# Optimization experiments

Hardware: AMD Instinct MI355X
Metric: run time of the kernel (lower is better)

Reference implementation:

```python
import jax, jax.numpy as jnp
import numpy as np

# Config: b=2, n=1024, dim=512, heads=8, dim_head=64, L=8 slices/head, temperature=0.1

def setup_inputs() -> dict:
    key = jax.random.key(0)
    ks = jax.random.split(key, 5)
    b, n, dim = 2, 1024, 512
    heads, dim_head, L = 8, 64, 8
    inner = heads * dim_head
    x = jax.random.normal(ks[0], (b, n, dim), jnp.float32)
    W_qkv = jax.random.normal(ks[1], (dim, 3 * inner), jnp.float32) * 0.02
    theta = jax.random.normal(ks[2], (heads, L, dim_head), jnp.float32)
    W_out = jax.random.normal(ks[3], (inner, dim), jnp.float32) * 0.02
    b_out = jnp.zeros((dim,), jnp.float32)
    return {"x": x, "W_qkv": W_qkv, "theta": theta, "W_out": W_out, "b_out": b_out}


def reference(x, W_qkv, theta, W_out, b_out):
    b, n, dim = x.shape
    heads, L, dim_head = theta.shape
    scale = dim_head ** -0.5
    temperature = 0.1
    # QKV projection (no bias) and head split: b n (h d) -> b h n d
    qkv = x @ W_qkv
    q, k, v = jnp.split(qkv, 3, axis=-1)
    sh = lambda t: t.reshape(b, n, heads, dim_head).transpose(0, 2, 1, 3)
    q = sh(q) * scale
    k = sh(k) * scale
    v = sh(v)
    # Esp: learnable unit slice directions per head, 1D projections
    th = theta / jnp.linalg.norm(theta, axis=-1, keepdims=True)  # [h, L, d]
    qp = jnp.einsum('bhnd,hld->bhln', q, th)  # [b,h,L,n]
    kp = jnp.einsum('bhnd,hld->bhln', k, th)
    # per-slice soft 1D transport plan (rows sum to 1), averaged over slices,
    # scaled to total-mass-1 plan (rows sum 1/n)
    d2 = (qp[..., :, None] - kp[..., None, :]) ** 2  # [b,h,L,n,n]
    plans = jax.nn.softmax(-d2 / temperature, axis=-1)
    P = plans.mean(axis=2) / n  # [b,h,n,n], rows sum to 1/n
    # SA: attn = attn * attn.shape[-1] -> row-stochastic
    attn = P * n
    out = jnp.einsum('bhnm,bhmd->bhnd', attn, v)
    out = out.transpose(0, 2, 1, 3).reshape(b, n, heads * dim_head)
    out = out @ W_out + b_out  # to_out Linear (dropout=0 in eval)
    return out, attn
```

## Files before the change

### kernel.cpp

```cpp
#include <hip/hip_runtime.h>
#include <hip/hip_bf16.h>

#define CEXP (-14.4269504088896340736f)

typedef __attribute__((ext_vector_type(8))) short bfrag8;
typedef __attribute__((ext_vector_type(4))) float fvec4;
typedef __attribute__((ext_vector_type(8))) unsigned short ushort8;
typedef __attribute__((ext_vector_type(4))) unsigned short ushort4v;

__device__ inline unsigned short f2bf(float f) {
    unsigned u = __builtin_bit_cast(unsigned, f);
    u += 0x7fffu + ((u >> 16) & 1u);
    return (unsigned short)(u >> 16);
}
__device__ inline float bf2f(unsigned short h) {
    unsigned u = ((unsigned)h) << 16;
    return __builtin_bit_cast(float, u);
}

template <int CTRL, int RMASK>
__device__ __forceinline__ float dpp_add(float v) {
    int m = __builtin_amdgcn_update_dpp(0, __builtin_bit_cast(int, v), CTRL, RMASK, 0xf, true);
    return v + __builtin_bit_cast(float, m);
}
__device__ __forceinline__ float wave_sum64(float v) {
    v = dpp_add<0xB1,  0xf>(v);
    v = dpp_add<0x4E,  0xf>(v);
    v = dpp_add<0x141, 0xf>(v);
    v = dpp_add<0x140, 0xf>(v);
    v = dpp_add<0x142, 0xa>(v);
    v = dpp_add<0x143, 0xc>(v);
    return __builtin_bit_cast(float, __builtin_amdgcn_readlane(__builtin_bit_cast(int, v), 63));
}

__global__ __launch_bounds__(256) void k_wproj(const float* __restrict__ Wqkv,
                                               const float* __restrict__ theta,
                                               const float* __restrict__ Wout,
                                               float* __restrict__ Wqp,
                                               float* __restrict__ Wkp,
                                               float* __restrict__ Wv,
                                               unsigned short* __restrict__ WoThi,
                                               unsigned short* __restrict__ WoTlo) {
    __shared__ float th_s[64 * 65];
    __shared__ float ts2[64 * 65];
    int tid = threadIdx.x;
    int hl = tid & 63, cl = tid >> 6;
    #pragma unroll
    for (int i = 0; i < 16; ++i) {
        int r = cl * 16 + i;
        th_s[r * 65 + hl] = theta[r * 64 + hl];
    }
    __syncthreads();
    const float* ts = th_s + hl * 65;
    float ss = 0.f;
    #pragma unroll 8
    for (int d = 0; d < 64; ++d) ss = fmaf(ts[d], ts[d], ss);
    float inv = rsqrtf(ss);
    int c = blockIdx.x * 4 + cl;
    int h = hl >> 3;
    const float* wq = Wqkv + c * 1536 + h * 64;
    const float* wk = wq + 512;
    float aq = 0.f, ak = 0.f;
    #pragma unroll 4
    for (int d = 0; d < 64; ++d) {
        float tv = ts[d];
        aq = fmaf(wq[d], tv, aq);
        ak = fmaf(wk[d], tv, ak);
    }
    Wqp[c * 64 + hl] = aq * inv;
    Wkp[c * 64 + hl] = ak * inv;

    int c0b = blockIdx.x * 4;
    const float4* src = (const float4*)(Wqkv + 1024);
    float4* dst = (float4*)Wv;
    #pragma unroll
    for (int j = 0; j < 2; ++j) {
        int idx = j * 256 + tid;
        int cr = c0b + (idx >> 7), o4 = idx & 127;
        dst[cr * 128 + o4] = src[cr * 384 + o4];
    }

    if (blockIdx.x < 64) {
        int r0 = (blockIdx.x >> 3) * 64;
        int c0 = (blockIdx.x & 7) * 64;
        int cc = tid & 63, rr = tid >> 6;
        #pragma unroll
        for (int k = 0; k < 16; ++k) {
            int r = rr + 4 * k;
            ts2[r * 65 + cc] = Wout[(r0 + r) * 512 + c0 + cc];
        }
        __syncthreads();
        int kk = tid & 63, nn = tid >> 6;
        #pragma unroll
        for (int i = 0; i < 16; ++i) {
            int n = nn + 4 * i;
            float v = ts2[kk * 65 + n];
            unsigned short hi = f2bf(v);
            WoThi[(size_t)(c0 + n) * 512 + r0 + kk] = hi;
            WoTlo[(size_t)(c0 + n) * 512 + r0 + kk] = f2bf(v - bf2f(hi));
        }
    }
}

__global__ __launch_bounds__(512) void k_proj(const float* __restrict__ x,
                                              const float* __restrict__ Wqp,
                                              const float* __restrict__ Wkp,
                                              const float* __restrict__ Wv,
                                              float* __restrict__ qp,
                                              float* __restrict__ kp,
                                              unsigned short* __restrict__ vThi,
                                              unsigned short* __restrict__ vTlo) {
    __shared__ float xs[8 * 512];
    __shared__ float combraw[4096];
    int tid = threadIdx.x;
    if (blockIdx.x < 512) {
        float (*comb)[128][4] = (float(*)[128][4])combraw;
        int i0 = blockIdx.x * 4;
        const float4* xg = (const float4*)(x + i0 * 512);
        ((float4*)xs)[tid] = xg[tid];
        __syncthreads();

        int t  = tid & 127;
        int kh = tid >> 7;
        int hl = t & 63;
        const float* Bm = (t & 64) ? Wkp : Wqp;
        float a[4] = {0.f, 0.f, 0.f, 0.f};
        int c4b = kh * 32;
        for (int c4 = c4b; c4 < c4b + 32; ++c4) {
            float b0 = Bm[(c4 * 4 + 0) * 64 + hl];
            float b1 = Bm[(c4 * 4 + 1) * 64 + hl];
            float b2 = Bm[(c4 * 4 + 2) * 64 + hl];
            float b3 = Bm[(c4 * 4 + 3) * 64 + hl];
            #pragma unroll
            for (int r = 0; r < 4; ++r) {
                float4 xv = *(const float4*)(xs + r * 512 + c4 * 4);
                a[r] = fmaf(xv.x, b0, fmaf(xv.y, b1, fmaf(xv.z, b2, fmaf(xv.w, b3, a[r]))));
            }
        }
        #pragma unroll
        for (int r = 0; r < 4; ++r) comb[kh][t][r] = a[r];
        __syncthreads();

        if (tid < 128) {
            int hl2 = tid & 63;
            int h = hl2 >> 3, l = hl2 & 7;
            float* dstp = (tid & 64) ? kp : qp;
            int b = i0 >> 10, i = i0 & 1023;
            fvec4 st;
            #pragma unroll
            for (int r = 0; r < 4; ++r)
                st[r] = (comb[0][tid][r] + comb[1][tid][r] + comb[2][tid][r] + comb[3][tid][r]) * 0.125f;
            *(fvec4*)(dstp + ((b * 8 + h) * 8 + l) * 1024 + i) = st;
        }
    } else {
        float (*comb)[256][8] = (float(*)[256][8])combraw;
        int blk2 = blockIdx.x - 512;
        int ch = blk2 & 1;
        int i0 = (blk2 >> 1) * 8;
        const float4* xg = (const float4*)(x + i0 * 512);
        #pragma unroll
        for (int j = 0; j < 2; ++j) ((float4*)xs)[j * 512 + tid] = xg[j * 512 + tid];
        __syncthreads();

        int t  = tid & 255;
        int kh = tid >> 8;
        int col = ch * 256 + t;
        const float* wp = Wv + col;
        float a[8];
        #pragma unroll
        for (int r = 0; r < 8; ++r) a[r] = 0.f;
        int c4b = kh * 64;
        for (int c4 = c4b; c4 < c4b + 64; ++c4) {
            float w0 = wp[(c4 * 4 + 0) * 512];
            float w1 = wp[(c4 * 4 + 1) * 512];
            float w2 = wp[(c4 * 4 + 2) * 512];
            float w3 = wp[(c4 * 4 + 3) * 512];
            #pragma unroll
            for (int r = 0; r < 8; ++r) {
                float4 xv = *(const float4*)(xs + r * 512 + c4 * 4);
                a[r] = fmaf(xv.x, w0, fmaf(xv.y, w1, fmaf(xv.z, w2, fmaf(xv.w, w3, a[r]))));
            }
        }
        #pragma unroll
        for (int r = 0; r < 8; ++r) comb[kh][t][r] = a[r];
        __syncthreads();

        if (tid < 256) {
            int col2 = ch * 256 + tid;
            int h = col2 >> 6, d = col2 & 63;
            int b = i0 >> 10, ib = i0 & 1023;
            ushort8 vh, vl;
            #pragma unroll
            for (int r = 0; r < 8; ++r) {
                float v = comb[0][tid][r] + comb[1][tid][r];
                unsigned short hi = f2bf(v);
                vh[r] = hi;
                vl[r] = f2bf(v - bf2f(hi));
            }
            size_t off = (size_t)(b * 8 + h) * 65536 + (size_t)d * 1024 + ib;
            *(ushort8*)(vThi + off) = vh;
            *(ushort8*)(vTlo + off) = vl;
        }
    }
}

__global__ __launch_bounds__(512) void k_attn_pv(const float* __restrict__ qp,
                                                 const float* __restrict__ kp,
                                                 const unsigned short* __restrict__ vThi,
                                                 const unsigned short* __restrict__ vTlo,
                                                 float* __restrict__ attn,
                                                 float* __restrict__ oh) {
    __shared__ float s_buf[8 * 1024];
    __shared__ float sc[4 * 64 * 4];
    int bx = blockIdx.x;
    int idx = bx >> 3;
    int bh = (bx & 7) * 2 + (idx >> 7);
    int rowbase = (idx & 127) * 8;
    int tid = threadIdx.x;
    int w = tid >> 6, lane = tid & 63;

    const float4* kp4 = (const float4*)(kp + bh * 8192);
    float4* kps4 = (float4*)s_buf;
    #pragma unroll
    for (int k = 0; k < 4; ++k) kps4[k * 512 + tid] = kp4[k * 512 + tid];

    int r = rowbase + w;
    float qv[8];
    #pragma unroll
    for (int l = 0; l < 8; ++l) qv[l] = qp[bh * 8192 + l * 1024 + r];
    __syncthreads();

    const fvec4 CE4 = {CEXP, CEXP, CEXP, CEXP};
    fvec4 acc4[4];
    #pragma unroll
    for (int mm = 0; mm < 4; ++mm) acc4[mm] = (fvec4){0.f, 0.f, 0.f, 0.f};

    for (int l = 0; l < 8; ++l) {
        fvec4 kv4[4], e4[4];
        #pragma unroll
        for (int mm = 0; mm < 4; ++mm)
            kv4[mm] = *(const fvec4*)(s_buf + l * 1024 + mm * 256 + lane * 4);
        float sqs = -2.f * CEXP * qv[l];
        fvec4 sq4 = {sqs, sqs, sqs, sqs};
        fvec4 sum4 = {0.f, 0.f, 0.f, 0.f};
        #pragma unroll
        for (int mm = 0; mm < 4; ++mm) {
            fvec4 k2 = (kv4[mm] * kv4[mm]) * CE4;
            fvec4 t  = sq4 * kv4[mm] + k2;
            fvec4 e;
            e[0] = __builtin_amdgcn_exp2f(t[0]);
            e[1] = __builtin_amdgcn_exp2f(t[1]);
            e[2] = __builtin_amdgcn_exp2f(t[2]);
            e[3] = __builtin_amdgcn_exp2f(t[3]);
            e4[mm] = e;
            sum4 += e;
        }
        float s = (sum4[0] + sum4[1]) + (sum4[2] + sum4[3]);
        float inv = 0.125f * __builtin_amdgcn_rcpf(wave_sum64(s));
        fvec4 inv4 = {inv, inv, inv, inv};
        #pragma unroll
        for (int mm = 0; mm < 4; ++mm) acc4[mm] = e4[mm] * inv4 + acc4[mm];
    }

    __syncthreads();

    unsigned short* ps = (unsigned short*)s_buf;
    int swz = w << 3;
    #pragma unroll
    for (int mm = 0; mm < 4; ++mm) {
        ushort4v h4, l4;
        #pragma unroll
        for (int jj = 0; jj < 4; ++jj) {
            float v = acc4[mm][jj];
            unsigned short hi = f2bf(v);
            h4[jj] = hi;
            l4[jj] = f2bf(v - bf2f(hi));
        }
        int j0 = mm * 256 + lane * 4;
        *(ushort4v*)(ps + w * 1024 + (j0 ^ swz))       = h4;
        *(ushort4v*)(ps + (w + 8) * 1024 + (j0 ^ swz)) = l4;
    }
    __syncthreads();

    float* aR = attn + ((size_t)(bh * 1024 + r)) * 1024;
    #pragma unroll
    for (int mm = 0; mm < 4; ++mm)
        *(fvec4*)(aR + mm * 256 + lane * 4) = acc4[mm];

    int n0 = (w & 3) * 16;
    int kh = w >> 2;
    int ar  = lane & 15;
    int asw = (ar & 7) << 3;
    int ak  = (lane >> 4) * 8;
    const unsigned short* ap = ps + ar * 1024;
    size_t boff = (size_t)bh * 65536 + (size_t)(n0 + (lane & 15)) * 1024 + ak;
    const unsigned short* bh_p = vThi + boff;
    const unsigned short* bl_p = vTlo + boff;
    fvec4 c2 = {0.f, 0.f, 0.f, 0.f};
    #pragma unroll 4
    for (int s = kh * 16; s < kh * 16 + 16; ++s) {
        bfrag8 a  = *(const bfrag8*)(ap + ((s * 32 + ak) ^ asw));
        bfrag8 vh = *(const bfrag8*)(bh_p + s * 32);
        bfrag8 vl = *(const bfrag8*)(bl_p + s * 32);
        c2 = __builtin_amdgcn_mfma_f32_16x16x32_bf16(a, vh, c2, 0, 0, 0);
        c2 = __builtin_amdgcn_mfma_f32_16x16x32_bf16(a, vl, c2, 0, 0, 0);
    }
    if (w >= 4) {
        #pragma unroll
        for (int q = 0; q < 4; ++q) sc[(w - 4) * 256 + lane * 4 + q] = c2[q];
    }
    __syncthreads();
    if (w < 4) {
        int b = bh >> 3, h = bh & 7;
        #pragma unroll
        for (int q = 0; q < 4; ++q) {
            float t = c2[q] + sc[w * 256 + lane * 4 + q];
            t += __shfl_xor(t, 32);
            if (lane < 32) {
                int row = rowbase + (lane >> 4) * 4 + q;
                oh[(b * 1024 + row) * 512 + h * 64 + n0 + (lane & 15)] = t;
            }
        }
    }
}

__global__ __launch_bounds__(256) void k_out(const float* __restrict__ oh,
                                             const unsigned short* __restrict__ WoThi,
                                             const unsigned short* __restrict__ WoTlo,
                                             const float* __restrict__ bout,
                                             float* __restrict__ out) {
    __shared__ unsigned short ps[32 * 512];
    int blk = blockIdx.x;
    int cs = blk & 3;
    int rg = blk >> 2;
    int tid = threadIdx.x;
    int w = tid >> 6, lane = tid & 63;

    const float4* og = (const float4*)(oh + (size_t)rg * 16 * 512);
    #pragma unroll
    for (int rep = 0; rep < 8; ++rep) {
        int idx = rep * 256 + tid;
        int row = idx >> 7, c4 = idx & 127;
        float4 v = og[idx];
        int swz = (row & 7) << 3;
        int cbase = c4 * 4;
        ushort4v h4, l4;
        float vv[4] = {v.x, v.y, v.z, v.w};
        #pragma unroll
        for (int jj = 0; jj < 4; ++jj) {
            unsigned short hi = f2bf(vv[jj]);
            h4[jj] = hi;
            l4[jj] = f2bf(vv[jj] - bf2f(hi));
        }
        *(ushort4v*)(ps + row * 512 + (cbase ^ swz))        = h4;
        *(ushort4v*)(ps + (row + 16) * 512 + (cbase ^ swz)) = l4;
    }
    __syncthreads();

    int ar  = lane & 15;
    int asw = (ar & 7) << 3;
    int ak  = (lane >> 4) * 8;
    const unsigned short* aph = ps + ar * 512;
    const unsigned short* apl = ps + (ar + 16) * 512;
    int colb = cs * 128 + w * 32;
    size_t b0 = (size_t)(colb + ar) * 512 + ak;
    size_t b1 = b0 + 16 * 512;
    fvec4 acc0 = {0.f, 0.f, 0.f, 0.f};
    fvec4 acc1 = {0.f, 0.f, 0.f, 0.f};
    #pragma unroll 4
    for (int s = 0; s < 16; ++s) {
        int ko = s * 32 + ak;
        bfrag8 ahi = *(const bfrag8*)(aph + (ko ^ asw));
        bfrag8 alo = *(const bfrag8*)(apl + (ko ^ asw));
        bfrag8 bh0 = *(const bfrag8*)(WoThi + b0 + s * 32);
        bfrag8 bl0 = *(const bfrag8*)(WoTlo + b0 + s * 32);
        bfrag8 bh1 = *(const bfrag8*)(WoThi + b1 + s * 32);
        bfrag8 bl1 = *(const bfrag8*)(WoTlo + b1 + s * 32);
        acc0 = __builtin_amdgcn_mfma_f32_16x16x32_bf16(ahi, bh0, acc0, 0, 0, 0);
        acc0 = __builtin_amdgcn_mfma_f32_16x16x32_bf16(ahi, bl0, acc0, 0, 0, 0);
        acc0 = __builtin_amdgcn_mfma_f32_16x16x32_bf16(alo, bh0, acc0, 0, 0, 0);
        acc1 = __builtin_amdgcn_mfma_f32_16x16x32_bf16(ahi, bh1, acc1, 0, 0, 0);
        acc1 = __builtin_amdgcn_mfma_f32_16x16x32_bf16(ahi, bl1, acc1, 0, 0, 0);
        acc1 = __builtin_amdgcn_mfma_f32_16x16x32_bf16(alo, bh1, acc1, 0, 0, 0);
    }
    int rowb = rg * 16 + (lane >> 4) * 4;
    int col0 = colb + ar;
    float bias0 = bout[col0], bias1 = bout[col0 + 16];
    #pragma unroll
    for (int q = 0; q < 4; ++q) {
        out[(rowb + q) * 512 + col0]      = acc0[q] + bias0;
        out[(rowb + q) * 512 + col0 + 16] = acc1[q] + bias1;
    }
}

extern "C" void kernel_launch(void* const* d_in, const int* in_sizes, int n_in,
                              void* d_out, int out_size, void* d_ws, size_t ws_size,
                              hipStream_t stream) {
    const float* x     = (const float*)d_in[0];
    const float* Wqkv  = (const float*)d_in[1];
    const float* theta = (const float*)d_in[2];
    const float* Wout  = (const float*)d_in[3];
    const float* bout  = (const float*)d_in[4];

    float* out  = (float*)d_out;
    float* attn = out + 2 * 1024 * 512;

    float* ws  = (float*)d_ws;
    float* Wqp = ws;
    float* Wkp = ws + 32768;
    float* qp  = ws + 65536;
    float* kp  = ws + 196608;
    unsigned short* vThi = (unsigned short*)(ws + 327680);
    unsigned short* vTlo = (unsigned short*)(ws + 851968);
    float* oh   = ws + 1376256;
    float* Wv   = ws + 2424832;
    unsigned short* WoThi = (unsigned short*)(ws + 2686976);
    unsigned short* WoTlo = (unsigned short*)(ws + 2818048);

    k_wproj   <<<128,  256, 0, stream>>>(Wqkv, theta, Wout, Wqp, Wkp, Wv, WoThi, WoTlo);
    k_proj    <<<1024, 512, 0, stream>>>(x, Wqp, Wkp, Wv, qp, kp, vThi, vTlo);
    k_attn_pv <<<2048, 512, 0, stream>>>(qp, kp, vThi, vTlo, attn, oh);
    k_out     <<<512,  256, 0, stream>>>(oh, WoThi, WoTlo, bout, out);
}
```

Measured before the change: 139.3 us.

## Move QKV projection onto bf16 split-precision MFMA with pre-split x and weights

Converts the projection kernel from scalar fp32 FMAs to bf16 hi/lo split MFMA (three products per tile), with x split in k_wproj and a new k_wsplit kernel that transposes and splits the projected weights. The aim is to cut the compute time of the projection stage. The attention write also switches to nontemporal stores to reduce cache pollution from the large attn output. In exchange it adds a kernel launch and extra workspace traffic for the split copies, and accuracy is slightly below fp32 because the lo*lo term is dropped.

```diff
diff --git a/kernel.cpp b/kernel.cpp
--- a/kernel.cpp
+++ b/kernel.cpp
@@ -36,11 +36,14 @@
 __global__ __launch_bounds__(256) void k_wproj(const float* __restrict__ Wqkv,
                                                const float* __restrict__ theta,
                                                const float* __restrict__ Wout,
+                                               const float* __restrict__ x,
                                                float* __restrict__ Wqp,
                                                float* __restrict__ Wkp,
                                                float* __restrict__ Wv,
                                                unsigned short* __restrict__ WoThi,
-                                               unsigned short* __restrict__ WoTlo) {
+                                               unsigned short* __restrict__ WoTlo,
+                                               unsigned short* __restrict__ xhi,
+                                               unsigned short* __restrict__ xlo) {
     __shared__ float th_s[64 * 65];
     __shared__ float ts2[64 * 65];
     int tid = threadIdx.x;
@@ -80,6 +83,26 @@
         dst[cr * 128 + o4] = src[cr * 384 + o4];
     }
 
+    {
+        const float4* x4 = (const float4*)x;
+        int base4 = blockIdx.x * 2048;
+        #pragma unroll
+        for (int j = 0; j < 8; ++j) {
+            int idx = base4 + j * 256 + tid;
+            float4 v = x4[idx];
+            float vv[4] = {v.x, v.y, v.z, v.w};
+            ushort4v h4, l4;
+            #pragma unroll
+            for (int jj = 0; jj < 4; ++jj) {
+                unsigned short hi = f2bf(vv[jj]);
+                h4[jj] = hi;
+                l4[jj] = f2bf(vv[jj] - bf2f(hi));
+            }
+            *(ushort4v*)(xhi + (size_t)idx * 4) = h4;
+            *(ushort4v*)(xlo + (size_t)idx * 4) = l4;
+        }
+    }
+
     if (blockIdx.x < 64) {
         int r0 = (blockIdx.x >> 3) * 64;
         int c0 = (blockIdx.x & 7) * 64;
@@ -102,104 +125,121 @@
     }
 }
 
-__global__ __launch_bounds__(512) void k_proj(const float* __restrict__ x,
-                                              const float* __restrict__ Wqp,
-                                              const float* __restrict__ Wkp,
-                                              const float* __restrict__ Wv,
+__global__ __launch_bounds__(256) void k_wsplit(const float* __restrict__ Wqp,
+                                                const float* __restrict__ Wkp,
+                                                const float* __restrict__ Wv,
+                                                unsigned short* __restrict__ WThi,
+                                                unsigned short* __restrict__ WTlo) {
+    __shared__ float ts[64 * 65];
+    int blk = blockIdx.x;
+    const float* src;
+    int ld, k0, nbase;
+    if (blk < 8)       { src = Wqp + blk * 64 * 64;       ld = 64;  k0 = blk * 64;       nbase = 0; }
+    else if (blk < 16) { src = Wkp + (blk - 8) * 64 * 64; ld = 64;  k0 = (blk - 8) * 64; nbase = 64; }
+    else {
+        int t = blk - 16, kt = t >> 3, nt = t & 7;
+        src = Wv + kt * 64 * 512 + nt * 64;  ld = 512; k0 = kt * 64; nbase = 128 + nt * 64;
+    }
+    int tid = threadIdx.x;
+    int cc = tid & 63, rr = tid >> 6;
+    #pragma unroll
+    for (int k = 0; k < 16; ++k) {
+        int r = rr + 4 * k;
+        ts[r * 65 + cc] = src[r * ld + cc];
+    }
+    __syncthreads();
+    int kk = tid & 63, nn = tid >> 6;
+    #pragma unroll
+    for (int i = 0; i < 16; ++i) {
+        int n = nn + 4 * i;
+        float v = ts[kk * 65 + n];
+        unsigned short hi = f2bf(v);
+        WThi[(size_t)(nbase + n) * 512 + k0 + kk] = hi;
+        WTlo[(size_t)(nbase + n) * 512 + k0 + kk] = f2bf(v - bf2f(hi));
+    }
+}
+
+__global__ __launch_bounds__(256) void k_proj(const unsigned short* __restrict__ xhi,
+                                              const unsigned short* __restrict__ xlo,
+                                              const unsigned short* __restrict__ WThi,
+                                              const unsigned short* __restrict__ WTlo,
                                               float* __restrict__ qp,
                                               float* __restrict__ kp,
                                               unsigned short* __restrict__ vThi,
                                               unsigned short* __restrict__ vTlo) {
-    __shared__ float xs[8 * 512];
-    __shared__ float combraw[4096];
+    __shared__ unsigned short ps[32 * 512];
+    int blk = blockIdx.x;
+    int cs = blk % 5;
+    int rg = blk / 5;
     int tid = threadIdx.x;
-    if (blockIdx.x < 512) {
-        float (*comb)[128][4] = (float(*)[128][4])combraw;
-        int i0 = blockIdx.x * 4;
-        const float4* xg = (const float4*)(x + i0 * 512);
-        ((float4*)xs)[tid] = xg[tid];
-        __syncthreads();
-
-        int t  = tid & 127;
-        int kh = tid >> 7;
-        int hl = t & 63;
-        const float* Bm = (t & 64) ? Wkp : Wqp;
-        float a[4] = {0.f, 0.f, 0.f, 0.f};
-        int c4b = kh * 32;
-        for (int c4 = c4b; c4 < c4b + 32; ++c4) {
-            float b0 = Bm[(c4 * 4 + 0) * 64 + hl];
-            float b1 = Bm[(c4 * 4 + 1) * 64 + hl];
-            float b2 = Bm[(c4 * 4 + 2) * 64 + hl];
-            float b3 = Bm[(c4 * 4 + 3) * 64 + hl];
+    int w = tid >> 6, lane = tid & 63;
+
+    const ushort8* xh8 = (const ushort8*)(xhi + (size_t)rg * 16 * 512);
+    const ushort8* xl8 = (const ushort8*)(xlo + (size_t)rg * 16 * 512);
+    #pragma unroll
+    for (int rep = 0; rep < 4; ++rep) {
+        int idx = rep * 256 + tid;
+        int row = idx >> 6, c8 = (idx & 63) * 8;
+        int swz = (row & 7) << 3;
+        *(ushort8*)(ps + row * 512 + (c8 ^ swz))        = xh8[idx];
+        *(ushort8*)(ps + (row + 16) * 512 + (c8 ^ swz)) = xl8[idx];
+    }
+    __syncthreads();
+
+    int ar  = lane & 15;
+    int asw = (ar & 7) << 3;
+    int ak  = (lane >> 4) * 8;
+    const unsigned short* aph = ps + ar * 512;
+    const unsigned short* apl = ps + (ar + 16) * 512;
+    int colb = cs * 128 + w * 32;
+    size_t b0 = (size_t)(colb + ar) * 512 + ak;
+    size_t b1 = b0 + 16 * 512;
+    fvec4 acc0 = {0.f, 0.f, 0.f, 0.f};
+    fvec4 acc1 = {0.f, 0.f, 0.f, 0.f};
+    #pragma unroll 4
+    for (int s = 0; s < 16; ++s) {
+        int ko = s * 32 + ak;
+        bfrag8 ahi = *(const bfrag8*)(aph + (ko ^ asw));
+        bfrag8 alo = *(const bfrag8*)(apl + (ko ^ asw));
+        bfrag8 bh0 = *(const bfrag8*)(WThi + b0 + s * 32);
+        bfrag8 bl0 = *(const bfrag8*)(WTlo + b0 + s * 32);
+        bfrag8 bh1 = *(const bfrag8*)(WThi + b1 + s * 32);
+        bfrag8 bl1 = *(const bfrag8*)(WTlo + b1 + s * 32);
+        acc0 = __builtin_amdgcn_mfma_f32_16x16x32_bf16(ahi, bh0, acc0, 0, 0, 0);
+        acc0 = __builtin_amdgcn_mfma_f32_16x16x32_bf16(ahi, bl0, acc0, 0, 0, 0);
+        acc0 = __builtin_amdgcn_mfma_f32_16x16x32_bf16(alo, bh0, acc0, 0, 0, 0);
+        acc1 = __builtin_amdgcn_mfma_f32_16x16x32_bf16(ahi, bh1, acc1, 0, 0, 0);
+        acc1 = __builtin_amdgcn_mfma_f32_16x16x32_bf16(ahi, bl1, acc1, 0, 0, 0);
+        acc1 = __builtin_amdgcn_mfma_f32_16x16x32_bf16(alo, bh1, acc1, 0, 0, 0);
+    }
+
+    int rowb = rg * 16 + (lane >> 4) * 4;
+    int b = rowb >> 10, n = rowb & 1023;
+    fvec4 accs[2] = {acc0, acc1};
+    #pragma unroll
+    for (int t = 0; t < 2; ++t) {
+        int col = colb + t * 16 + ar;
+        fvec4 a = accs[t];
+        if (col < 128) {
+            int hl = col & 63;
+            float* dstp = (col < 64) ? qp : kp;
+            fvec4 st;
+            st[0] = a[0] * 0.125f; st[1] = a[1] * 0.125f;
+            st[2] = a[2] * 0.125f; st[3] = a[3] * 0.125f;
+            *(fvec4*)(dstp + ((size_t)((b * 8 + (hl >> 3)) * 8 + (hl & 7))) * 1024 + n) = st;
+        } else {
+            int vcol = col - 128;
+            int h = vcol >> 6, d = vcol & 63;
+            ushort4v h4, l4;
             #pragma unroll
-            for (int r = 0; r < 4; ++r) {
-                float4 xv = *(const float4*)(xs + r * 512 + c4 * 4);
-                a[r] = fmaf(xv.x, b0, fmaf(xv.y, b1, fmaf(xv.z, b2, fmaf(xv.w, b3, a[r]))));
+            for (int q = 0; q < 4; ++q) {
+                unsigned short hi = f2bf(a[q]);
+                h4[q] = hi;
+                l4[q] = f2bf(a[q] - bf2f(hi));
             }
-        }
-        #pragma unroll
-        for (int r = 0; r < 4; ++r) comb[kh][t][r] = a[r];
-        __syncthreads();
-
-        if (tid < 128) {
-            int hl2 = tid & 63;
-            int h = hl2 >> 3, l = hl2 & 7;
-            float* dstp = (tid & 64) ? kp : qp;
-            int b = i0 >> 10, i = i0 & 1023;
-            fvec4 st;
-            #pragma unroll
-            for (int r = 0; r < 4; ++r)
-                st[r] = (comb[0][tid][r] + comb[1][tid][r] + comb[2][tid][r] + comb[3][tid][r]) * 0.125f;
-            *(fvec4*)(dstp + ((b * 8 + h) * 8 + l) * 1024 + i) = st;
-        }
-    } else {
-        float (*comb)[256][8] = (float(*)[256][8])combraw;
-        int blk2 = blockIdx.x - 512;
-        int ch = blk2 & 1;
-        int i0 = (blk2 >> 1) * 8;
-        const float4* xg = (const float4*)(x + i0 * 512);
-        #pragma unroll
-        for (int j = 0; j < 2; ++j) ((float4*)xs)[j * 512 + tid] = xg[j * 512 + tid];
-        __syncthreads();
-
-        int t  = tid & 255;
-        int kh = tid >> 8;
-        int col = ch * 256 + t;
-        const float* wp = Wv + col;
-        float a[8];
-        #pragma unroll
-        for (int r = 0; r < 8; ++r) a[r] = 0.f;
-        int c4b = kh * 64;
-        for (int c4 = c4b; c4 < c4b + 64; ++c4) {
-            float w0 = wp[(c4 * 4 + 0) * 512];
-            float w1 = wp[(c4 * 4 + 1) * 512];
-            float w2 = wp[(c4 * 4 + 2) * 512];
-            float w3 = wp[(c4 * 4 + 3) * 512];
-            #pragma unroll
-            for (int r = 0; r < 8; ++r) {
-                float4 xv = *(const float4*)(xs + r * 512 + c4 * 4);
-                a[r] = fmaf(xv.x, w0, fmaf(xv.y, w1, fmaf(xv.z, w2, fmaf(xv.w, w3, a[r]))));
-            }
-        }
-        #pragma unroll
-        for (int r = 0; r < 8; ++r) comb[kh][t][r] = a[r];
-        __syncthreads();
-
-        if (tid < 256) {
-            int col2 = ch * 256 + tid;
-            int h = col2 >> 6, d = col2 & 63;
-            int b = i0 >> 10, ib = i0 & 1023;
-            ushort8 vh, vl;
-            #pragma unroll
-            for (int r = 0; r < 8; ++r) {
-                float v = comb[0][tid][r] + comb[1][tid][r];
-                unsigned short hi = f2bf(v);
-                vh[r] = hi;
-                vl[r] = f2bf(v - bf2f(hi));
-            }
-            size_t off = (size_t)(b * 8 + h) * 65536 + (size_t)d * 1024 + ib;
-            *(ushort8*)(vThi + off) = vh;
-            *(ushort8*)(vTlo + off) = vl;
+            size_t off = (size_t)(b * 8 + h) * 65536 + (size_t)d * 1024 + n;
+            *(ushort4v*)(vThi + off) = h4;
+            *(ushort4v*)(vTlo + off) = l4;
         }
     }
 }
@@ -285,7 +325,7 @@
     float* aR = attn + ((size_t)(bh * 1024 + r)) * 1024;
     #pragma unroll
     for (int mm = 0; mm < 4; ++mm)
-        *(fvec4*)(aR + mm * 256 + lane * 4) = acc4[mm];
+        __builtin_nontemporal_store(acc4[mm], (fvec4*)(aR + mm * 256 + lane * 4));
 
     int n0 = (w & 3) * 16;
     int kh = w >> 2;
@@ -413,12 +453,17 @@
     unsigned short* vThi = (unsigned short*)(ws + 327680);
     unsigned short* vTlo = (unsigned short*)(ws + 851968);
     float* oh   = ws + 1376256;
+    unsigned short* xhi = (unsigned short*)(ws + 1376256);
+    unsigned short* xlo = (unsigned short*)(ws + 1900544);
     float* Wv   = ws + 2424832;
     unsigned short* WoThi = (unsigned short*)(ws + 2686976);
     unsigned short* WoTlo = (unsigned short*)(ws + 2818048);
-
-    k_wproj   <<<128,  256, 0, stream>>>(Wqkv, theta, Wout, Wqp, Wkp, Wv, WoThi, WoTlo);
-    k_proj    <<<1024, 512, 0, stream>>>(x, Wqp, Wkp, Wv, qp, kp, vThi, vTlo);
+    unsigned short* WThi  = (unsigned short*)(ws + 2949120);
+    unsigned short* WTlo  = (unsigned short*)(ws + 3112960);
+
+    k_wproj   <<<128,  256, 0, stream>>>(Wqkv, theta, Wout, x, Wqp, Wkp, Wv, WoThi, WoTlo, xhi, xlo);
+    k_wsplit  <<<80,   256, 0, stream>>>(Wqp, Wkp, Wv, WThi, WTlo);
+    k_proj    <<<640,  256, 0, stream>>>(xhi, xlo, WThi, WTlo, qp, kp, vThi, vTlo);
     k_attn_pv <<<2048, 512, 0, stream>>>(qp, kp, vThi, vTlo, attn, oh);
     k_out     <<<512,  256, 0, stream>>>(oh, WoThi, WoTlo, bout, out);
 }
```

After: 131.7 us. 5.5% less time.
